# Optimization experiments

Hardware: AMD Instinct MI355X
Metric: run time of the kernel (lower is better)

Reference implementation:

```python
import jax, jax.numpy as jnp
import numpy as np

B, N, F, D = 8, 2048, 128, 128


def setup_inputs() -> dict:
    key = jax.random.key(0)
    k1, k2, k3 = jax.random.split(key, 3)
    inputs = jax.random.normal(k1, (B, N, F), dtype=jnp.float32)
    adj = jax.random.uniform(k2, (B, N, N), dtype=jnp.float32)  # nonneg weights -> positive degrees
    W_kernel = jax.random.normal(k3, (F, D), dtype=jnp.float32) * (1.0 / np.sqrt(F))
    W_bias = jnp.zeros((D,), dtype=jnp.float32)
    return {"inputs": inputs, "adj": adj, "W_kernel": W_kernel, "W_bias": W_bias}


def _normalize_adjacency(adj):
    # D^{-1/2} A D^{-1/2}: same math as diag-matmul chain, via broadcast scaling
    d = jnp.sum(adj, axis=-1)                      # [B, N]
    d_sqrt_inv = jnp.power(d, -0.5)
    d_sqrt_inv = jnp.where(jnp.isinf(d_sqrt_inv), 0.0, d_sqrt_inv)
    return d_sqrt_inv[..., :, None] * adj * d_sqrt_inv[..., None, :]


def reference(inputs, adj, W_kernel, W_bias):
    adj_norm = _normalize_adjacency(adj)           # [B, N, N]
    feats = inputs @ W_kernel + W_bias             # [B, N, D]
    out = jnp.einsum('bnm,bmd->bnd', adj_norm, feats)
    return jax.nn.relu(out)
```

## Files before the change

### kernel.cpp

```cpp
#include <hip/hip_runtime.h>
#include <hip/hip_bf16.h>
#include <stdint.h>

#define B_ 8
#define N_ 2048
#define F_ 128
#define D_ 128

typedef short bf16x8 __attribute__((ext_vector_type(8)));
typedef float f32x4 __attribute__((ext_vector_type(4)));

__device__ __forceinline__ unsigned short f2bf(float f) {
    unsigned u = __float_as_uint(f);
    u += 0x7fffu + ((u >> 16) & 1u);
    return (unsigned short)(u >> 16);
}

__global__ __launch_bounds__(256) void k_degfeat(const float* __restrict__ adj,
                                                 const float* __restrict__ x,
                                                 const float* __restrict__ W,
                                                 const float* __restrict__ bias,
                                                 float* __restrict__ rs,
                                                 unsigned short* __restrict__ gt) {
    __shared__ __align__(16) unsigned char sX[64 * 128 * 2];
    __shared__ __align__(16) unsigned char sW[128 * 128 * 2];

    const int t = threadIdx.x;
    if (blockIdx.x >= 256) {
        const int wave = t >> 6, lane = t & 63;
        const int row = (blockIdx.x - 256) * 4 + wave;
        const float4* p = (const float4*)(adj + (size_t)row * N_);
        float s = 0.f;
#pragma unroll
        for (int j = 0; j < 8; ++j) {
            float4 v = p[j * 64 + lane];
            s += (v.x + v.y) + (v.z + v.w);
        }
#pragma unroll
        for (int m = 1; m < 64; m <<= 1) s += __shfl_xor(s, m, 64);
        if (lane == 0) rs[row] = (s > 0.f) ? (1.0f / sqrtf(s)) : 0.f;
        return;
    }

    const int R0 = blockIdx.x * 64;

#pragma unroll
    for (int i = 0; i < 16; ++i) {
        int c = i * 256 + t;
        int f = c >> 5, d0 = (c & 31) * 4;
        float4 v = *(const float4*)(W + (size_t)f * D_ + d0);
        float vv[4] = {v.x, v.y, v.z, v.w};
#pragma unroll
        for (int e = 0; e < 4; ++e) {
            int dd = d0 + e;
            unsigned byte = (unsigned)(dd * 256 + f * 2);
            byte ^= ((byte >> 8) & 15u) << 4;
            *(unsigned short*)(sW + byte) = f2bf(vv[e]);
        }
    }
#pragma unroll
    for (int j = 0; j < 4; ++j) {
        int c = j * 256 + t;
        int row = c >> 4, sub = c & 15;
        const float4* src = (const float4*)(x + (size_t)(R0 + row) * F_ + sub * 8);
        float4 v0 = src[0], v1 = src[1];
        union { bf16x8 v; unsigned short u[8]; } pk;
        pk.u[0] = f2bf(v0.x); pk.u[1] = f2bf(v0.y); pk.u[2] = f2bf(v0.z); pk.u[3] = f2bf(v0.w);
        pk.u[4] = f2bf(v1.x); pk.u[5] = f2bf(v1.y); pk.u[6] = f2bf(v1.z); pk.u[7] = f2bf(v1.w);
        unsigned byte = (unsigned)(row * 256 + sub * 16);
        byte ^= ((byte >> 8) & 7u) << 4;
        *(bf16x8*)(sX + byte) = pk.v;
    }
    __syncthreads();

    const int w = t >> 6, l = t & 63, lr = l & 15, lh = l >> 4;
    f32x4 acc[8];
#pragma unroll
    for (int j = 0; j < 8; ++j) acc[j] = (f32x4){0.f, 0.f, 0.f, 0.f};

#pragma unroll
    for (int ks = 0; ks < 4; ++ks) {
        unsigned abyte = (unsigned)((w * 16 + lr) * 256 + lh * 16 + ks * 64);
        abyte ^= ((abyte >> 8) & 7u) << 4;
        bf16x8 a = *(const bf16x8*)(sX + abyte);
#pragma unroll
        for (int j = 0; j < 8; ++j) {
            unsigned bbyte = (unsigned)((j * 16 + lr) * 256 + lh * 16 + ks * 64);
            bbyte ^= ((bbyte >> 8) & 15u) << 4;
            bf16x8 bb = *(const bf16x8*)(sW + bbyte);
            acc[j] = __builtin_amdgcn_mfma_f32_16x16x32_bf16(a, bb, acc[j], 0, 0, 0);
        }
    }

#pragma unroll
    for (int j = 0; j < 8; ++j) {
        int d = j * 16 + lr;
        float bv = bias[d];
#pragma unroll
        for (int r = 0; r < 4; ++r) {
            int m = R0 + w * 16 + lh * 4 + r;
            int b = m >> 11, n = m & (N_ - 1);
            gt[((size_t)b * D_ + d) * N_ + n] = f2bf(acc[j][r] + bv);
        }
    }
}

__global__ __launch_bounds__(512) void k_gcn(const float* __restrict__ adj,
                                             const unsigned short* __restrict__ gt,
                                             const float* __restrict__ rs,
                                             float* __restrict__ out) {
    __shared__ __align__(16) unsigned char sA[2][64 * 256];
    __shared__ __align__(16) unsigned char sB[2][128 * 256];
    __shared__ __align__(16) float sRS[N_];

    unsigned bid = blockIdx.x;
    unsigned wg = (bid & 7u) * 32u + (bid >> 3);
    const int b = (int)(wg >> 5);
    const int R0 = (int)(wg & 31u) * 64;

    const float* adjB = adj + (size_t)b * N_ * N_ + (size_t)R0 * N_;
    const unsigned short* gtB = gt + (size_t)b * D_ * N_;
    const float* rsB = rs + (size_t)b * N_;

    const int t = threadIdx.x;
    const int w = t >> 6, l = t & 63, lr = l & 15, lh = l >> 4;
    const int wr = w >> 2, wc = w & 3;

    const unsigned short* bSrc[4];
    unsigned bL[4];
#pragma unroll
    for (int i = 0; i < 4; ++i) {
        unsigned c = (unsigned)(i * 512 + t);
        unsigned L = c * 16u;
        unsigned lg = L ^ (((L >> 8) & 7u) << 4);
        bL[i] = L;
        bSrc[i] = gtB + (size_t)(lg >> 8) * N_ + ((lg & 255u) >> 1);
    }
    auto issueB = [&](int buf, int k0) {
        unsigned char* pB = sB[buf];
#pragma unroll
        for (int i = 0; i < 4; ++i) {
            __builtin_amdgcn_global_load_lds(
                (const __attribute__((address_space(1))) void*)(bSrc[i] + k0),
                (__attribute__((address_space(3))) void*)(pB + bL[i]), 16, 0, 0);
        }
    };

    const float* aSrc = adjB + (size_t)(t >> 3) * N_ + (t & 7) * 16;
    const unsigned aRow = (unsigned)(t >> 3);
    const unsigned aBase = aRow * 256u + (unsigned)((t & 7) * 32);
    const unsigned aSwz = (aRow & 7u) << 4;
    const int rsIdx0 = (t & 7) * 4;

    f32x4 acc[2][2];
#pragma unroll
    for (int i = 0; i < 2; ++i)
#pragma unroll
        for (int jn = 0; jn < 2; ++jn) acc[i][jn] = (f32x4){0.f, 0.f, 0.f, 0.f};

    __builtin_amdgcn_global_load_lds(
        (const __attribute__((address_space(1))) void*)((const unsigned char*)rsB + t * 16),
        (__attribute__((address_space(3))) void*)((unsigned char*)sRS + t * 16), 16, 0, 0);
    issueB(0, 0);
    f32x4 aA[4];
#pragma unroll
    for (int j = 0; j < 4; ++j) aA[j] = *(const f32x4*)(aSrc + j * 4);
    asm volatile("s_waitcnt vmcnt(8)" ::: "memory");
    __builtin_amdgcn_s_barrier();

    const int NITER = N_ / 128;
    for (int it = 0; it < NITER; ++it) {
        const int cur = it & 1;
        f32x4 nA[4];
#pragma unroll
        for (int j = 0; j < 4; ++j) nA[j] = aA[j];
        if (it + 1 < NITER) {
            issueB(cur ^ 1, (it + 1) * 128);
            const float* s = aSrc + (it + 1) * 128;
#pragma unroll
            for (int j = 0; j < 4; ++j) nA[j] = *(const f32x4*)(s + j * 4);
            asm volatile("s_waitcnt vmcnt(8)" ::: "memory");
        } else {
            asm volatile("s_waitcnt vmcnt(0)" ::: "memory");
        }
        __builtin_amdgcn_sched_barrier(0);

        {
            const f32x4* rsV = (const f32x4*)sRS + (it * 32 + rsIdx0);
            unsigned u[8];
#pragma unroll
            for (int j = 0; j < 4; ++j) {
                f32x4 xj = aA[j] * rsV[j];
                asm("v_cvt_pk_bf16_f32 %0, %1, %2" : "=v"(u[2 * j]) : "v"(xj[0]), "v"(xj[1]));
                asm("v_cvt_pk_bf16_f32 %0, %1, %2" : "=v"(u[2 * j + 1]) : "v"(xj[2]), "v"(xj[3]));
            }
            union { unsigned u[4]; bf16x8 v; } p0, p1;
            p0.u[0] = u[0]; p0.u[1] = u[1]; p0.u[2] = u[2]; p0.u[3] = u[3];
            p1.u[0] = u[4]; p1.u[1] = u[5]; p1.u[2] = u[6]; p1.u[3] = u[7];
            *(bf16x8*)(sA[cur] + (aBase ^ aSwz)) = p0.v;
            *(bf16x8*)(sA[cur] + ((aBase + 16) ^ aSwz)) = p1.v;
        }
        asm volatile("s_waitcnt lgkmcnt(0)" ::: "memory");
        __builtin_amdgcn_sched_barrier(0);
        __builtin_amdgcn_s_barrier();

        const unsigned char* pA = sA[cur];
        const unsigned char* pB = sB[cur];
#pragma unroll
        for (int kk = 0; kk < 4; ++kk) {
            bf16x8 a[2], bb[2];
#pragma unroll
            for (int i = 0; i < 2; ++i) {
                unsigned row = (unsigned)(wr * 32 + i * 16 + lr);
                unsigned byte = row * 256 + (unsigned)(kk * 64 + lh * 16);
                byte ^= (row & 7u) << 4;
                a[i] = *(const bf16x8*)(pA + byte);
            }
#pragma unroll
            for (int jn = 0; jn < 2; ++jn) {
                unsigned d = (unsigned)(wc * 32 + jn * 16 + lr);
                unsigned byte = d * 256 + (unsigned)(kk * 64 + lh * 16);
                byte ^= (d & 7u) << 4;
                bb[jn] = *(const bf16x8*)(pB + byte);
            }
#pragma unroll
            for (int i = 0; i < 2; ++i)
#pragma unroll
                for (int jn = 0; jn < 2; ++jn)
                    acc[i][jn] = __builtin_amdgcn_mfma_f32_16x16x32_bf16(a[i], bb[jn], acc[i][jn], 0, 0, 0);
        }
        __builtin_amdgcn_s_barrier();

#pragma unroll
        for (int j = 0; j < 4; ++j) aA[j] = nA[j];
    }

#pragma unroll
    for (int i = 0; i < 2; ++i) {
#pragma unroll
        for (int r = 0; r < 4; ++r) {
            int rowl = wr * 32 + i * 16 + lh * 4 + r;
            float rsn = sRS[R0 + rowl];
#pragma unroll
            for (int jn = 0; jn < 2; ++jn) {
                int d = wc * 32 + jn * 16 + lr;
                float v = acc[i][jn][r] * rsn;
                out[((size_t)(b * N_ + R0 + rowl)) * D_ + d] = fmaxf(v, 0.f);
            }
        }
    }
}

extern "C" void kernel_launch(void* const* d_in, const int* in_sizes, int n_in,
                              void* d_out, int out_size, void* d_ws, size_t ws_size,
                              hipStream_t stream) {
    const float* inputs = (const float*)d_in[0];
    const float* adj    = (const float*)d_in[1];
    const float* Wk     = (const float*)d_in[2];
    const float* Wb     = (const float*)d_in[3];
    float* out = (float*)d_out;

    float* rs = (float*)d_ws;
    unsigned short* gt = (unsigned short*)((char*)d_ws + 65536);

    k_degfeat<<<256 + 4096, 256, 0, stream>>>(adj, inputs, Wk, Wb, rs, gt);
    k_gcn    <<<256, 512, 0, stream>>>(adj, gt, rs, out);
}
```

Baseline: 62.09 us.

## Fuse degree/feature kernel into GCN kernel with per-batch flag synchronization

Merges the degree-sum and feature-projection kernel into the main GCN matmul kernel as a single cooperative launch of 256 blocks. Each block computes its own slice of the projected features and row-normalization factors, publishes a release flag, and spins until all 32 tiles of its batch are ready. This removes a kernel launch boundary and lets blocks of one batch move on without waiting for the whole grid. The cost is an extra memset, spin-wait traffic, and the projection and degree work now running at one-block-per-CU occupancy, where before it was spread over many small blocks.

```diff
diff --git a/kernel.cpp b/kernel.cpp
--- a/kernel.cpp
+++ b/kernel.cpp
@@ -16,114 +16,118 @@
     return (unsigned short)(u >> 16);
 }
 
-__global__ __launch_bounds__(256) void k_degfeat(const float* __restrict__ adj,
-                                                 const float* __restrict__ x,
-                                                 const float* __restrict__ W,
-                                                 const float* __restrict__ bias,
-                                                 float* __restrict__ rs,
-                                                 unsigned short* __restrict__ gt) {
-    __shared__ __align__(16) unsigned char sX[64 * 128 * 2];
-    __shared__ __align__(16) unsigned char sW[128 * 128 * 2];
+__global__ __launch_bounds__(512, 1) void k_fused(const float* __restrict__ adj,
+                                                  const float* __restrict__ x,
+                                                  const float* __restrict__ W,
+                                                  const float* __restrict__ bias,
+                                                  float* __restrict__ rs,
+                                                  unsigned short* __restrict__ gt,
+                                                  unsigned int* __restrict__ flags,
+                                                  float* __restrict__ out) {
+    __shared__ __align__(16) unsigned char lds[104 * 1024];
+    unsigned char* sX = lds;
+    unsigned char* sW = lds + 16 * 1024;
+    float* sRS = (float*)(lds + 96 * 1024);
 
     const int t = threadIdx.x;
-    if (blockIdx.x >= 256) {
-        const int wave = t >> 6, lane = t & 63;
-        const int row = (blockIdx.x - 256) * 4 + wave;
-        const float4* p = (const float4*)(adj + (size_t)row * N_);
-        float s = 0.f;
-#pragma unroll
-        for (int j = 0; j < 8; ++j) {
-            float4 v = p[j * 64 + lane];
-            s += (v.x + v.y) + (v.z + v.w);
-        }
-#pragma unroll
-        for (int m = 1; m < 64; m <<= 1) s += __shfl_xor(s, m, 64);
-        if (lane == 0) rs[row] = (s > 0.f) ? (1.0f / sqrtf(s)) : 0.f;
-        return;
-    }
-
-    const int R0 = blockIdx.x * 64;
-
-#pragma unroll
-    for (int i = 0; i < 16; ++i) {
-        int c = i * 256 + t;
-        int f = c >> 5, d0 = (c & 31) * 4;
-        float4 v = *(const float4*)(W + (size_t)f * D_ + d0);
-        float vv[4] = {v.x, v.y, v.z, v.w};
-#pragma unroll
-        for (int e = 0; e < 4; ++e) {
-            int dd = d0 + e;
-            unsigned byte = (unsigned)(dd * 256 + f * 2);
-            byte ^= ((byte >> 8) & 15u) << 4;
-            *(unsigned short*)(sW + byte) = f2bf(vv[e]);
-        }
-    }
-#pragma unroll
-    for (int j = 0; j < 4; ++j) {
-        int c = j * 256 + t;
-        int row = c >> 4, sub = c & 15;
-        const float4* src = (const float4*)(x + (size_t)(R0 + row) * F_ + sub * 8);
-        float4 v0 = src[0], v1 = src[1];
-        union { bf16x8 v; unsigned short u[8]; } pk;
-        pk.u[0] = f2bf(v0.x); pk.u[1] = f2bf(v0.y); pk.u[2] = f2bf(v0.z); pk.u[3] = f2bf(v0.w);
-        pk.u[4] = f2bf(v1.x); pk.u[5] = f2bf(v1.y); pk.u[6] = f2bf(v1.z); pk.u[7] = f2bf(v1.w);
-        unsigned byte = (unsigned)(row * 256 + sub * 16);
-        byte ^= ((byte >> 8) & 7u) << 4;
-        *(bf16x8*)(sX + byte) = pk.v;
-    }
-    __syncthreads();
-
-    const int w = t >> 6, l = t & 63, lr = l & 15, lh = l >> 4;
-    f32x4 acc[8];
-#pragma unroll
-    for (int j = 0; j < 8; ++j) acc[j] = (f32x4){0.f, 0.f, 0.f, 0.f};
-
-#pragma unroll
-    for (int ks = 0; ks < 4; ++ks) {
-        unsigned abyte = (unsigned)((w * 16 + lr) * 256 + lh * 16 + ks * 64);
-        abyte ^= ((abyte >> 8) & 7u) << 4;
-        bf16x8 a = *(const bf16x8*)(sX + abyte);
-#pragma unroll
-        for (int j = 0; j < 8; ++j) {
-            unsigned bbyte = (unsigned)((j * 16 + lr) * 256 + lh * 16 + ks * 64);
-            bbyte ^= ((bbyte >> 8) & 15u) << 4;
-            bf16x8 bb = *(const bf16x8*)(sW + bbyte);
-            acc[j] = __builtin_amdgcn_mfma_f32_16x16x32_bf16(a, bb, acc[j], 0, 0, 0);
-        }
-    }
-
-#pragma unroll
-    for (int j = 0; j < 8; ++j) {
-        int d = j * 16 + lr;
-        float bv = bias[d];
-#pragma unroll
-        for (int r = 0; r < 4; ++r) {
-            int m = R0 + w * 16 + lh * 4 + r;
-            int b = m >> 11, n = m & (N_ - 1);
-            gt[((size_t)b * D_ + d) * N_ + n] = f2bf(acc[j][r] + bv);
-        }
-    }
-}
-
-__global__ __launch_bounds__(512) void k_gcn(const float* __restrict__ adj,
-                                             const unsigned short* __restrict__ gt,
-                                             const float* __restrict__ rs,
-                                             float* __restrict__ out) {
-    __shared__ __align__(16) unsigned char sA[2][64 * 256];
-    __shared__ __align__(16) unsigned char sB[2][128 * 256];
-    __shared__ __align__(16) float sRS[N_];
-
-    unsigned bid = blockIdx.x;
-    unsigned wg = (bid & 7u) * 32u + (bid >> 3);
-    const int b = (int)(wg >> 5);
-    const int R0 = (int)(wg & 31u) * 64;
+    const int bid = blockIdx.x;
+    const int b = bid & 7;
+    const int nt = bid >> 3;
+    const int R0 = nt * 64;
 
     const float* adjB = adj + (size_t)b * N_ * N_ + (size_t)R0 * N_;
     const unsigned short* gtB = gt + (size_t)b * D_ * N_;
     const float* rsB = rs + (size_t)b * N_;
 
-    const int t = threadIdx.x;
     const int w = t >> 6, l = t & 63, lr = l & 15, lh = l >> 4;
+
+    {
+#pragma unroll
+        for (int i = 0; i < 8; ++i) {
+            int c = i * 512 + t;
+            int f = c >> 5, d0 = (c & 31) * 4;
+            float4 v = *(const float4*)(W + (size_t)f * D_ + d0);
+            float vv[4] = {v.x, v.y, v.z, v.w};
+#pragma unroll
+            for (int e = 0; e < 4; ++e) {
+                int dd = d0 + e;
+                unsigned byte = (unsigned)(dd * 256 + f * 2);
+                byte ^= ((byte >> 8) & 15u) << 4;
+                *(unsigned short*)(sW + byte) = f2bf(vv[e]);
+            }
+        }
+#pragma unroll
+        for (int j = 0; j < 2; ++j) {
+            int c = j * 512 + t;
+            int row = c >> 4, sub = c & 15;
+            const float4* src = (const float4*)(x + (size_t)(b * N_ + R0 + row) * F_ + sub * 8);
+            float4 v0 = src[0], v1 = src[1];
+            union { bf16x8 v; unsigned short u[8]; } pk;
+            pk.u[0] = f2bf(v0.x); pk.u[1] = f2bf(v0.y); pk.u[2] = f2bf(v0.z); pk.u[3] = f2bf(v0.w);
+            pk.u[4] = f2bf(v1.x); pk.u[5] = f2bf(v1.y); pk.u[6] = f2bf(v1.z); pk.u[7] = f2bf(v1.w);
+            unsigned byte = (unsigned)(row * 256 + sub * 16);
+            byte ^= ((byte >> 8) & 7u) << 4;
+            *(bf16x8*)(sX + byte) = pk.v;
+        }
+        __syncthreads();
+
+        const int rw = w & 3, ch = w >> 2;
+        f32x4 acc4[4];
+#pragma unroll
+        for (int j = 0; j < 4; ++j) acc4[j] = (f32x4){0.f, 0.f, 0.f, 0.f};
+#pragma unroll
+        for (int ks = 0; ks < 4; ++ks) {
+            unsigned abyte = (unsigned)((rw * 16 + lr) * 256 + lh * 16 + ks * 64);
+            abyte ^= ((abyte >> 8) & 7u) << 4;
+            bf16x8 a = *(const bf16x8*)(sX + abyte);
+#pragma unroll
+            for (int j = 0; j < 4; ++j) {
+                int d = ch * 64 + j * 16 + lr;
+                unsigned bbyte = (unsigned)(d * 256 + lh * 16 + ks * 64);
+                bbyte ^= ((bbyte >> 8) & 15u) << 4;
+                bf16x8 bb = *(const bf16x8*)(sW + bbyte);
+                acc4[j] = __builtin_amdgcn_mfma_f32_16x16x32_bf16(a, bb, acc4[j], 0, 0, 0);
+            }
+        }
+        const int m0 = R0 + rw * 16 + lh * 4;
+#pragma unroll
+        for (int j = 0; j < 4; ++j) {
+            int d = ch * 64 + j * 16 + lr;
+            float bv = bias[d];
+#pragma unroll
+            for (int r = 0; r < 4; ++r)
+                gt[((size_t)b * D_ + d) * N_ + m0 + r] = f2bf(acc4[j][r] + bv);
+        }
+    }
+
+    {
+#pragma unroll 2
+        for (int rr = 0; rr < 8; ++rr) {
+            int row = R0 + w * 8 + rr;
+            const float4* p = (const float4*)(adj + (size_t)(b * N_ + row) * N_);
+            float s = 0.f;
+#pragma unroll
+            for (int j = 0; j < 8; ++j) {
+                float4 v = p[j * 64 + l];
+                s += (v.x + v.y) + (v.z + v.w);
+            }
+#pragma unroll
+            for (int m = 1; m < 64; m <<= 1) s += __shfl_xor(s, m, 64);
+            if (l == 0) rs[b * N_ + row] = (s > 0.f) ? (1.0f / sqrtf(s)) : 0.f;
+        }
+    }
+    __syncthreads();
+    if (t == 0)
+        __hip_atomic_store(&flags[b * 32 + nt], 1u, __ATOMIC_RELEASE, __HIP_MEMORY_SCOPE_AGENT);
+
+    if (t < 32) {
+        while (__hip_atomic_load(&flags[b * 32 + t], __ATOMIC_ACQUIRE, __HIP_MEMORY_SCOPE_AGENT) == 0u)
+            __builtin_amdgcn_s_sleep(2);
+    }
+    __syncthreads();
+
+    unsigned char* sA0 = lds;
+    unsigned char* sB0 = lds + 32 * 1024;
     const int wr = w >> 2, wc = w & 3;
 
     const unsigned short* bSrc[4];
@@ -137,7 +141,7 @@
         bSrc[i] = gtB + (size_t)(lg >> 8) * N_ + ((lg & 255u) >> 1);
     }
     auto issueB = [&](int buf, int k0) {
-        unsigned char* pB = sB[buf];
+        unsigned char* pB = sB0 + buf * 32 * 1024;
 #pragma unroll
         for (int i = 0; i < 4; ++i) {
             __builtin_amdgcn_global_load_lds(
@@ -197,15 +201,16 @@
             union { unsigned u[4]; bf16x8 v; } p0, p1;
             p0.u[0] = u[0]; p0.u[1] = u[1]; p0.u[2] = u[2]; p0.u[3] = u[3];
             p1.u[0] = u[4]; p1.u[1] = u[5]; p1.u[2] = u[6]; p1.u[3] = u[7];
-            *(bf16x8*)(sA[cur] + (aBase ^ aSwz)) = p0.v;
-            *(bf16x8*)(sA[cur] + ((aBase + 16) ^ aSwz)) = p1.v;
+            unsigned char* pA = sA0 + cur * 16 * 1024;
+            *(bf16x8*)(pA + (aBase ^ aSwz)) = p0.v;
+            *(bf16x8*)(pA + ((aBase + 16) ^ aSwz)) = p1.v;
         }
         asm volatile("s_waitcnt lgkmcnt(0)" ::: "memory");
         __builtin_amdgcn_sched_barrier(0);
         __builtin_amdgcn_s_barrier();
 
-        const unsigned char* pA = sA[cur];
-        const unsigned char* pB = sB[cur];
+        const unsigned char* pA = sA0 + cur * 16 * 1024;
+        const unsigned char* pB = sB0 + cur * 32 * 1024;
 #pragma unroll
         for (int kk = 0; kk < 4; ++kk) {
             bf16x8 a[2], bb[2];
@@ -262,7 +267,11 @@
 
     float* rs = (float*)d_ws;
     unsigned short* gt = (unsigned short*)((char*)d_ws + 65536);
-
-    k_degfeat<<<256 + 4096, 256, 0, stream>>>(adj, inputs, Wk, Wb, rs, gt);
-    k_gcn    <<<256, 512, 0, stream>>>(adj, gt, rs, out);
+    unsigned int* flags = (unsigned int*)((char*)d_ws + 65536 + (size_t)B_ * D_ * N_ * 2);
+
+    hipMemsetAsync(flags, 0, 1024, stream);
+
+    void* args[] = {(void*)&adj, (void*)&inputs, (void*)&Wk, (void*)&Wb,
+                    (void*)&rs, (void*)&gt, (void*)&flags, (void*)&out};
+    hipLaunchCooperativeKernel((void*)k_fused, dim3(256), dim3(512), args, 0, stream);
 }
```

After: 93.90 us. +51.2%, slower.
